# Kernel optimization log

Hardware: AMD Instinct MI355X
Metric: run time of the kernel (lower is better)

The kernel has to match this reference:

```python
import jax, jax.numpy as jnp
import numpy as np

N, E, P = 50000, 800000, 500000
NODE_IN, HIDDEN, EDGE_IN = 128, 256, 16


def setup_inputs() -> dict:
    key = jax.random.key(0)
    ks = jax.random.split(key, 16)
    s = lambda k, shape, fan_in: jax.random.normal(k, shape, jnp.float32) * (1.0 / np.sqrt(fan_in))
    return {
        "x": jax.random.normal(ks[0], (N, NODE_IN), jnp.float32),
        "edge_index": jax.random.randint(ks[1], (2, E), 0, N),
        "edge_u": jax.random.randint(ks[2], (P,), 0, N),
        "edge_v": jax.random.randint(ks[3], (P,), 0, N),
        "edge_attr": jax.random.normal(ks[4], (P, EDGE_IN), jnp.float32),
        "log_exposure": jax.random.normal(ks[5], (P,), jnp.float32),
        # conv1: lin_l (on mean-aggregated neighbors, with bias), lin_r (on root, no bias)
        "Wl1": s(ks[6], (HIDDEN, NODE_IN), NODE_IN),
        "bl1": jnp.zeros((HIDDEN,), jnp.float32),
        "Wr1": s(ks[7], (HIDDEN, NODE_IN), NODE_IN),
        # conv2
        "Wl2": s(ks[8], (HIDDEN, HIDDEN), HIDDEN),
        "bl2": jnp.zeros((HIDDEN,), jnp.float32),
        "Wr2": s(ks[9], (HIDDEN, HIDDEN), HIDDEN),
        # edge MLP: Linear(2*hidden+edge_in, hidden) -> ReLU -> Linear(hidden, 1)
        "W1": s(ks[10], (HIDDEN, 2 * HIDDEN + EDGE_IN), 2 * HIDDEN + EDGE_IN),
        "b1": jnp.zeros((HIDDEN,), jnp.float32),
        "W2": s(ks[11], (1, HIDDEN), HIDDEN),
        "b2": jnp.zeros((1,), jnp.float32),
    }


def sage_conv(x, src, dst, Wl, bl, Wr):
    # PyG SAGEConv, mean aggregation: out = lin_l(mean_{j in N(i)} x_j) + lin_r(x_i)
    n = x.shape[0]
    agg = jax.ops.segment_sum(x[src], dst, num_segments=n)          # [N, F]
    cnt = jax.ops.segment_sum(jnp.ones((src.shape[0],), x.dtype), dst, num_segments=n)
    agg = agg / jnp.maximum(cnt, 1.0)[:, None]
    return agg @ Wl.T + bl + x @ Wr.T


def reference(x, edge_index, edge_u, edge_v, edge_attr, log_exposure,
              Wl1, bl1, Wr1, Wl2, bl2, Wr2, W1, b1, W2, b2):
    src, dst = edge_index[0], edge_index[1]
    # eval mode: dropout is identity
    h = jax.nn.relu(sage_conv(x, src, dst, Wl1, bl1, Wr1))
    h = jax.nn.relu(sage_conv(h, src, dst, Wl2, bl2, Wr2))
    z = jnp.concatenate([h[edge_u], h[edge_v], edge_attr], axis=1)  # [P, 2H+Ein]
    s = (jax.nn.relu(z @ W1.T + b1) @ W2.T + b2)[:, 0]              # [P]
    return log_exposure + s
```

## Files before the change

kernel.cpp:

```cpp
#include <hip/hip_runtime.h>


typedef float f32x4 __attribute__((ext_vector_type(4)));
typedef float f32x2 __attribute__((ext_vector_type(2)));
typedef __bf16 bf16x8 __attribute__((ext_vector_type(8)));

__device__ __forceinline__ unsigned short f2b(float f) {
    unsigned u = __float_as_uint(f);
    u = u + 0x7fffu + ((u >> 16) & 1u);
    return (unsigned short)(u >> 16);
}
__device__ __forceinline__ float b2f(unsigned short s) {
    return __uint_as_float(((unsigned)s) << 16);
}
__device__ __forceinline__ int swz(int r, int g) { return (g + (r >> 1)) & 3; }
__device__ __forceinline__ unsigned char f2f8(float v) {
    return (unsigned char)(__builtin_amdgcn_cvt_pk_fp8_f32(v, v, 0, false) & 0xff);
}


__global__ void k_count(const int* __restrict__ dst, int* __restrict__ cnt, int E) {
    int e = blockIdx.x * 256 + threadIdx.x;
    if (e < E) atomicAdd(&cnt[dst[e]], 1);
}

__global__ __launch_bounds__(1024) void k_scan(int* __restrict__ cnt_cursor,
                                               int* __restrict__ row_ptr, int n) {
    __shared__ int wsum[16];
    __shared__ int carry, wtot;
    int t = threadIdx.x, lane = t & 63, w = t >> 6;
    if (t == 0) carry = 0;
    __syncthreads();
    int nch = (n + 1023) >> 10;
    for (int ch = 0; ch < nch; ++ch) {
        int i = (ch << 10) + t;
        int v = (i < n) ? cnt_cursor[i] : 0;
        int s = v;
        #pragma unroll
        for (int off = 1; off < 64; off <<= 1) {
            int u = __shfl_up(s, off);
            if (lane >= off) s += u;
        }
        if (lane == 63) wsum[w] = s;
        __syncthreads();
        if (t < 16) {
            int vv = wsum[t];
            int s2 = vv;
            #pragma unroll
            for (int off = 1; off < 16; off <<= 1) {
                int u = __shfl_up(s2, off);
                if (t >= off) s2 += u;
            }
            wsum[t] = s2 - vv;
            if (t == 15) wtot = s2;
        }
        __syncthreads();
        int base = carry;
        int incl = s + wsum[w];
        if (i < n) { int ex = base + incl - v; row_ptr[i] = ex; cnt_cursor[i] = ex; }
        __syncthreads();
        if (t == 0) carry = base + wtot;
    }
    __syncthreads();
    if (t == 0) row_ptr[n] = carry;
}

__global__ void k_scatter(const int* __restrict__ src, const int* __restrict__ dst,
                          int* __restrict__ cursor, int* __restrict__ bucket, int E) {
    int e = blockIdx.x * 256 + threadIdx.x;
    if (e < E) {
        int p = atomicAdd(&cursor[dst[e]], 1);
        bucket[p] = src[e];
    }
}


__global__ void k_convert_weights(const float* __restrict__ Wl1, const float* __restrict__ Wr1,
                                  const float* __restrict__ Wl2, const float* __restrict__ Wr2,
                                  const float* __restrict__ W1, const float* __restrict__ b1,
                                  unsigned short* __restrict__ Wc1,
                                  unsigned short* __restrict__ Wc2,
                                  unsigned short* __restrict__ W1g,
                                  unsigned short* __restrict__ WaF) {
    int idx = blockIdx.x * 256 + threadIdx.x;
    if (idx < 65536) {
        int c = idx >> 13, j = (idx >> 5) & 255, kk = idx & 31;
        float v = (c < 4) ? Wl1[j * 128 + c * 32 + kk] : Wr1[j * 128 + (c - 4) * 32 + kk];
        Wc1[idx] = f2b(v);
    } else if (idx < 65536 + 131072) {
        int i2 = idx - 65536;
        int c = i2 >> 13, j = (i2 >> 5) & 255, kk = i2 & 31;
        float v = (c < 8) ? Wl2[j * 256 + c * 32 + kk] : Wr2[j * 256 + (c - 8) * 32 + kk];
        Wc2[i2] = f2b(v);
    } else if (idx < 65536 + 131072 + 131072) {
        int i3 = idx - 65536 - 131072;
        int c = i3 >> 14, j = (i3 >> 5) & 511, kk = i3 & 31;
        float v = (j < 256) ? W1[(size_t)j * 528 + c * 32 + kk]
                            : W1[(size_t)(j - 256) * 528 + 256 + c * 32 + kk];
        W1g[i3] = f2b(v);
    } else if (idx < 65536 + 131072 + 131072 + 8192) {
        int i4 = idx - 65536 - 131072 - 131072;
        int mi = i4 >> 9, l = (i4 >> 3) & 63, j = i4 & 7;
        int m = mi * 16 + (l & 15);
        int k = (l >> 4) * 8 + j;
        float v = (k < 16) ? W1[(size_t)m * 528 + 512 + k] : (k == 16 ? b1[m] : 0.f);
        WaF[i4] = f2b(v);
    }
}

__global__ void k_xconvert(const float* __restrict__ in, unsigned short* __restrict__ xb,
                           unsigned char* __restrict__ xf8, int n) {
    int j = (blockIdx.x * 256 + threadIdx.x) * 2;
    if (j < n) {
        float a = in[j], b = in[j + 1];
        xb[j] = f2b(a); xb[j + 1] = f2b(b);
        unsigned p = __builtin_amdgcn_cvt_pk_fp8_f32(a, b, 0, false);
        *reinterpret_cast<unsigned short*>(xf8 + j) = (unsigned short)(p & 0xffffu);
    }
}


__device__ __forceinline__ void accf8(uint2 v, float* s) {
    f32x2 p0 = __builtin_amdgcn_cvt_pk_f32_fp8(v.x, false);
    f32x2 p1 = __builtin_amdgcn_cvt_pk_f32_fp8(v.x, true);
    f32x2 p2 = __builtin_amdgcn_cvt_pk_f32_fp8(v.y, false);
    f32x2 p3 = __builtin_amdgcn_cvt_pk_f32_fp8(v.y, true);
    s[0] += p0.x; s[1] += p0.y; s[2] += p1.x; s[3] += p1.y;
    s[4] += p2.x; s[5] += p2.y; s[6] += p3.x; s[7] += p3.y;
}

__global__ __launch_bounds__(256) void k_agg_x(const unsigned char* __restrict__ xf8,
                                               const int* __restrict__ row_ptr,
                                               const int* __restrict__ bucket,
                                               unsigned short* __restrict__ agg, int Nn) {
    int node = blockIdx.x * 4 + (threadIdx.x >> 6);
    if (node >= Nn) return;
    int lane = threadIdx.x & 63;
    int q = lane >> 4, c = lane & 15;
    int beg = row_ptr[node], end = row_ptr[node + 1];
    int len = end - beg;
    int lo = beg + ((len * q) >> 2);
    int hi = beg + ((len * (q + 1)) >> 2);
    float s[8] = {0.f,0.f,0.f,0.f,0.f,0.f,0.f,0.f};
    const unsigned char* xp = xf8 + c * 8;
    int e = lo;
    for (; e + 4 <= hi; e += 4) {
        int b0 = bucket[e], b1 = bucket[e + 1], b2 = bucket[e + 2], b3 = bucket[e + 3];
        uint2 v0 = *reinterpret_cast<const uint2*>(xp + (size_t)b0 * 128);
        uint2 v1 = *reinterpret_cast<const uint2*>(xp + (size_t)b1 * 128);
        uint2 v2 = *reinterpret_cast<const uint2*>(xp + (size_t)b2 * 128);
        uint2 v3 = *reinterpret_cast<const uint2*>(xp + (size_t)b3 * 128);
        accf8(v0, s); accf8(v1, s); accf8(v2, s); accf8(v3, s);
    }
    for (; e < hi; ++e)
        accf8(*reinterpret_cast<const uint2*>(xp + (size_t)bucket[e] * 128), s);
    #pragma unroll
    for (int j = 0; j < 8; ++j) {
        s[j] += __shfl_xor(s[j], 16);
        s[j] += __shfl_xor(s[j], 32);
    }
    if (q == 0) {
        float sc = 1.0f / (float)(len > 1 ? len : 1);
        uint4 o;
        o.x = (unsigned)f2b(s[0]*sc) | ((unsigned)f2b(s[1]*sc) << 16);
        o.y = (unsigned)f2b(s[2]*sc) | ((unsigned)f2b(s[3]*sc) << 16);
        o.z = (unsigned)f2b(s[4]*sc) | ((unsigned)f2b(s[5]*sc) << 16);
        o.w = (unsigned)f2b(s[6]*sc) | ((unsigned)f2b(s[7]*sc) << 16);
        *reinterpret_cast<uint4*>(agg + (size_t)node * 128 + c * 8) = o;
    }
}

__global__ __launch_bounds__(256) void k_agg_h(const unsigned char* __restrict__ hf8,
                                               const int* __restrict__ row_ptr,
                                               const int* __restrict__ bucket,
                                               unsigned short* __restrict__ agg, int Nn) {
    int node = blockIdx.x * 4 + (threadIdx.x >> 6);
    if (node >= Nn) return;
    int lane = threadIdx.x & 63;
    int g = lane >> 5, c = lane & 31;
    int beg = row_ptr[node], end = row_ptr[node + 1];
    int len = end - beg;
    int lo = beg + ((len * g) >> 1);
    int hi = beg + ((len * (g + 1)) >> 1);
    float s[8] = {0.f,0.f,0.f,0.f,0.f,0.f,0.f,0.f};
    const unsigned char* hp = hf8 + c * 8;
    int e = lo;
    for (; e + 4 <= hi; e += 4) {
        int b0 = bucket[e], b1 = bucket[e + 1], b2 = bucket[e + 2], b3 = bucket[e + 3];
        uint2 v0 = *reinterpret_cast<const uint2*>(hp + (size_t)b0 * 256);
        uint2 v1 = *reinterpret_cast<const uint2*>(hp + (size_t)b1 * 256);
        uint2 v2 = *reinterpret_cast<const uint2*>(hp + (size_t)b2 * 256);
        uint2 v3 = *reinterpret_cast<const uint2*>(hp + (size_t)b3 * 256);
        accf8(v0, s); accf8(v1, s); accf8(v2, s); accf8(v3, s);
    }
    for (; e < hi; ++e)
        accf8(*reinterpret_cast<const uint2*>(hp + (size_t)bucket[e] * 256), s);
    #pragma unroll
    for (int j = 0; j < 8; ++j) s[j] += __shfl_xor(s[j], 32);
    if (g == 0) {
        float sc = 1.0f / (float)(len > 1 ? len : 1);
        uint4 o;
        o.x = (unsigned)f2b(s[0]*sc) | ((unsigned)f2b(s[1]*sc) << 16);
        o.y = (unsigned)f2b(s[2]*sc) | ((unsigned)f2b(s[3]*sc) << 16);
        o.z = (unsigned)f2b(s[4]*sc) | ((unsigned)f2b(s[5]*sc) << 16);
        o.w = (unsigned)f2b(s[6]*sc) | ((unsigned)f2b(s[7]*sc) << 16);
        *reinterpret_cast<uint4*>(agg + (size_t)node * 256 + c * 8) = o;
    }
}


__global__ __launch_bounds__(256) void k_conv_gemm(const unsigned short* __restrict__ Aagg,
                                                   const unsigned short* __restrict__ Aself,
                                                   const unsigned short* __restrict__ Wck,
                                                   const float* __restrict__ bias,
                                                   unsigned short* __restrict__ Hout,
                                                   unsigned char* __restrict__ Hf8,
                                                   int Nn, int F) {
    __shared__ __align__(16) unsigned short zt[128 * 32];
    __shared__ __align__(16) unsigned short wt[128 * 32];
    const int t = threadIdx.x;
    const int lane = t & 63, w = t >> 6;
    const int wm = w >> 1, wn = w & 1;
    const int node0 = blockIdx.x * 128;
    const int colh = blockIdx.y;
    const int half = F >> 5, nchunks = F >> 4;

    f32x4 acc[4][4];
    #pragma unroll
    for (int i = 0; i < 4; ++i)
        #pragma unroll
        for (int j = 0; j < 4; ++j) acc[i][j] = (f32x4){0.f, 0.f, 0.f, 0.f};

    for (int c = 0; c < nchunks; ++c) {
        __syncthreads();
        const unsigned short* Asrc = (c < half) ? Aagg : Aself;
        const int ccol = ((c < half) ? c : c - half) * 32;
        #pragma unroll
        for (int p = 0; p < 2; ++p) {
            int fc = t + p * 256;
            int row = fc >> 2, seg = fc & 3;
            int node = node0 + row; if (node >= Nn) node = Nn - 1;
            uint4 v = *reinterpret_cast<const uint4*>(Asrc + (size_t)node * F + ccol + seg * 8);
            *reinterpret_cast<uint4*>(&zt[row * 32 + swz(row, seg) * 8]) = v;
        }
        const unsigned short* Wsrc = Wck + ((size_t)c * 256 + colh * 128) * 32;
        #pragma unroll
        for (int p = 0; p < 2; ++p) {
            int fc = t + p * 256;
            int row = fc >> 2, seg = fc & 3;
            *reinterpret_cast<uint4*>(&wt[row * 32 + swz(row, seg) * 8]) =
                *reinterpret_cast<const uint4*>(Wsrc + fc * 8);
        }
        __syncthreads();
        bf16x8 a[4], b[4];
        const int q = lane >> 4;
        #pragma unroll
        for (int mi = 0; mi < 4; ++mi) {
            int R = wm * 64 + mi * 16 + (lane & 15);
            a[mi] = *reinterpret_cast<const bf16x8*>(&zt[R * 32 + swz(R, q) * 8]);
        }
        #pragma unroll
        for (int ni = 0; ni < 4; ++ni) {
            int R = wn * 64 + ni * 16 + (lane & 15);
            b[ni] = *reinterpret_cast<const bf16x8*>(&wt[R * 32 + swz(R, q) * 8]);
        }
        #pragma unroll
        for (int mi = 0; mi < 4; ++mi)
            #pragma unroll
            for (int ni = 0; ni < 4; ++ni)
                acc[mi][ni] = __builtin_amdgcn_mfma_f32_16x16x32_bf16(a[mi], b[ni], acc[mi][ni], 0, 0, 0);
    }

    #pragma unroll
    for (int mi = 0; mi < 4; ++mi)
        #pragma unroll
        for (int ni = 0; ni < 4; ++ni) {
            int col = colh * 128 + wn * 64 + ni * 16 + (lane & 15);
            float bia = bias[col];
            #pragma unroll
            for (int r = 0; r < 4; ++r) {
                int row = node0 + wm * 64 + mi * 16 + ((lane >> 4) << 2) + r;
                if (row < Nn) {
                    float v = acc[mi][ni][r] + bia;
                    v = v > 0.f ? v : 0.f;
                    Hout[(size_t)row * 256 + col] = f2b(v);
                    if (Hf8) Hf8[(size_t)row * 256 + col] = f2f8(v);
                }
            }
        }
}


__global__ __launch_bounds__(256) void k_gemm_g(const unsigned short* __restrict__ A,
                                                const unsigned short* __restrict__ Wck,
                                                unsigned char* __restrict__ Gout,
                                                int Nn) {
    __shared__ __align__(16) unsigned short zt[128 * 32];
    __shared__ __align__(16) unsigned short wt[128 * 32];
    const int t = threadIdx.x;
    const int lane = t & 63, w = t >> 6;
    const int wm = w >> 1, wn = w & 1;
    const int node0 = blockIdx.x * 128;
    const int colg = blockIdx.y;

    f32x4 acc[4][4];
    #pragma unroll
    for (int i = 0; i < 4; ++i)
        #pragma unroll
        for (int j = 0; j < 4; ++j) acc[i][j] = (f32x4){0.f, 0.f, 0.f, 0.f};

    for (int c = 0; c < 8; ++c) {
        __syncthreads();
        #pragma unroll
        for (int p = 0; p < 2; ++p) {
            int fc = t + p * 256;
            int row = fc >> 2, seg = fc & 3;
            int node = node0 + row; if (node >= Nn) node = Nn - 1;
            uint4 v = *reinterpret_cast<const uint4*>(A + (size_t)node * 256 + c * 32 + seg * 8);
            *reinterpret_cast<uint4*>(&zt[row * 32 + swz(row, seg) * 8]) = v;
        }
        const unsigned short* Wsrc = Wck + ((size_t)c * 512 + colg * 128) * 32;
        #pragma unroll
        for (int p = 0; p < 2; ++p) {
            int fc = t + p * 256;
            int row = fc >> 2, seg = fc & 3;
            *reinterpret_cast<uint4*>(&wt[row * 32 + swz(row, seg) * 8]) =
                *reinterpret_cast<const uint4*>(Wsrc + fc * 8);
        }
        __syncthreads();
        bf16x8 a[4], b[4];
        const int q = lane >> 4;
        #pragma unroll
        for (int mi = 0; mi < 4; ++mi) {
            int R = wm * 64 + mi * 16 + (lane & 15);
            a[mi] = *reinterpret_cast<const bf16x8*>(&zt[R * 32 + swz(R, q) * 8]);
        }
        #pragma unroll
        for (int ni = 0; ni < 4; ++ni) {
            int R = wn * 64 + ni * 16 + (lane & 15);
            b[ni] = *reinterpret_cast<const bf16x8*>(&wt[R * 32 + swz(R, q) * 8]);
        }
        #pragma unroll
        for (int mi = 0; mi < 4; ++mi)
            #pragma unroll
            for (int ni = 0; ni < 4; ++ni)
                acc[mi][ni] = __builtin_amdgcn_mfma_f32_16x16x32_bf16(a[mi], b[ni], acc[mi][ni], 0, 0, 0);
    }

    #pragma unroll
    for (int mi = 0; mi < 4; ++mi)
        #pragma unroll
        for (int ni = 0; ni < 4; ++ni) {
            int col = colg * 128 + wn * 64 + ni * 16 + (lane & 15);
            #pragma unroll
            for (int r = 0; r < 4; ++r) {
                int row = node0 + wm * 64 + mi * 16 + ((lane >> 4) << 2) + r;
                if (row < Nn)
                    Gout[(size_t)row * 512 + col] = f2f8(acc[mi][ni][r]);
            }
        }
}


__global__ __launch_bounds__(256, 6) void k_edge(const unsigned char* __restrict__ G2,
                                                 const float* __restrict__ attr,
                                                 const int* __restrict__ eu,
                                                 const int* __restrict__ ev,
                                                 const uint4* __restrict__ WaF,
                                                 const float* __restrict__ W2,
                                                 const float* __restrict__ b2,
                                                 const float* __restrict__ logexp,
                                                 float* __restrict__ out, int P) {
    __shared__ __align__(16) unsigned short attrT[64 * 40];
    __shared__ __align__(16) unsigned char gt[64 * 264];
    __shared__ float w2s[256];
    __shared__ int euv[128];
    const int t = threadIdx.x;
    const int lane = t & 63, w = t >> 6;
    const int base = blockIdx.x * 64;

    {
        int e = t >> 2, seg = t & 3;
        int eg = base + e; if (eg >= P) eg = P - 1;
        const float4 f = *reinterpret_cast<const float4*>(attr + (size_t)eg * 16 + seg * 4);
        uint2 o;
        o.x = (unsigned)f2b(f.x) | ((unsigned)f2b(f.y) << 16);
        o.y = (unsigned)f2b(f.z) | ((unsigned)f2b(f.w) << 16);
        *reinterpret_cast<uint2*>(&attrT[e * 40 + seg * 4]) = o;
    }
    if (t < 64) {
        uint2 z0; z0.x = 0x3f80u; z0.y = 0u;
        *reinterpret_cast<uint2*>(&attrT[t * 40 + 16]) = z0;
        uint2 z1; z1.x = 0u; z1.y = 0u;
        *reinterpret_cast<uint2*>(&attrT[t * 40 + 20]) = z1;
        uint4 z2; z2.x = z2.y = z2.z = z2.w = 0u;
        *reinterpret_cast<uint4*>(&attrT[t * 40 + 24]) = z2;
    }
    if (t < 128) {
        int e = t >> 1;
        int eg = base + e; if (eg >= P) eg = P - 1;
        euv[t] = (t & 1) ? ev[eg] : eu[eg];
    }
    w2s[t] = W2[t];
    __syncthreads();

    const int el = lane & 15, q = lane >> 4;
    const int grow = w * 16 + el;
    const bf16x8 bfrag = *reinterpret_cast<const bf16x8*>(&attrT[grow * 40 + q * 8]);

    float s = 0.f;
    #pragma unroll
    for (int p = 0; p < 2; ++p) {
        {
            const int sub = lane >> 4, c = lane & 15;
            #pragma unroll
            for (int i = 0; i < 4; ++i) {
                int le = w * 16 + i * 4 + sub;
                int u = euv[2 * le], v = euv[2 * le + 1];
                uint2 a = *reinterpret_cast<const uint2*>(G2 + (size_t)u * 512 + p * 128 + c * 8);
                uint2 b = *reinterpret_cast<const uint2*>(G2 + (size_t)v * 512 + 256 + p * 128 + c * 8);
                *reinterpret_cast<uint2*>(&gt[le * 264 + c * 8]) = a;
                *reinterpret_cast<uint2*>(&gt[le * 264 + 128 + c * 8]) = b;
            }
        }
        #pragma unroll
        for (int m = 0; m < 8; ++m) {
            const int mi = p * 8 + m;
            const bf16x8 af = *reinterpret_cast<const bf16x8*>(&WaF[mi * 64 + lane]);
            f32x4 acc = __builtin_amdgcn_mfma_f32_16x16x32_bf16(af, bfrag, (f32x4){0.f,0.f,0.f,0.f}, 0, 0, 0);
            const unsigned gu4 = *reinterpret_cast<const unsigned*>(&gt[grow * 264 + m * 16 + q * 4]);
            const unsigned gv4 = *reinterpret_cast<const unsigned*>(&gt[grow * 264 + 128 + m * 16 + q * 4]);
            const float4 w2v = *reinterpret_cast<const float4*>(&w2s[mi * 16 + q * 4]);
            f32x2 ulo = __builtin_amdgcn_cvt_pk_f32_fp8(gu4, false);
            f32x2 uhi = __builtin_amdgcn_cvt_pk_f32_fp8(gu4, true);
            f32x2 vlo = __builtin_amdgcn_cvt_pk_f32_fp8(gv4, false);
            f32x2 vhi = __builtin_amdgcn_cvt_pk_f32_fp8(gv4, true);
            float y0 = acc[0] + ulo.x + vlo.x;
            float y1 = acc[1] + ulo.y + vlo.y;
            float y2 = acc[2] + uhi.x + vhi.x;
            float y3 = acc[3] + uhi.y + vhi.y;
            s += (y0 > 0.f ? y0 : 0.f) * w2v.x;
            s += (y1 > 0.f ? y1 : 0.f) * w2v.y;
            s += (y2 > 0.f ? y2 : 0.f) * w2v.z;
            s += (y3 > 0.f ? y3 : 0.f) * w2v.w;
        }
        if (p == 0) __syncthreads();
    }
    s += __shfl_xor(s, 16);
    s += __shfl_xor(s, 32);
    int eg = base + grow;
    if (q == 0 && eg < P)
        out[eg] = logexp[eg] + b2[0] + s;
}


extern "C" void kernel_launch(void* const* d_in, const int* in_sizes, int n_in,
                              void* d_out, int out_size, void* d_ws, size_t ws_size,
                              hipStream_t stream) {
    const float* x      = (const float*)d_in[0];
    const int*   eidx   = (const int*)d_in[1];
    const int*   eu     = (const int*)d_in[2];
    const int*   ev     = (const int*)d_in[3];
    const float* attr   = (const float*)d_in[4];
    const float* logexp = (const float*)d_in[5];
    const float* Wl1    = (const float*)d_in[6];
    const float* bl1    = (const float*)d_in[7];
    const float* Wr1    = (const float*)d_in[8];
    const float* Wl2    = (const float*)d_in[9];
    const float* bl2    = (const float*)d_in[10];
    const float* Wr2    = (const float*)d_in[11];
    const float* W1     = (const float*)d_in[12];
    const float* b1     = (const float*)d_in[13];
    const float* W2     = (const float*)d_in[14];
    const float* b2     = (const float*)d_in[15];
    float* out = (float*)d_out;

    const int N = in_sizes[0] / 128;
    const int E = in_sizes[1] / 2;
    const int P = in_sizes[2];
    const int* src = eidx;
    const int* dst = eidx + E;

    char* ws = (char*)d_ws;
    size_t off = 0;
    auto alloc = [&](size_t bytes) -> void* {
        off = (off + 255) & ~(size_t)255;
        void* p = ws + off;
        off += bytes;
        return p;
    };
    int* row_ptr = (int*)alloc((size_t)(N + 1) * 4);
    int* cursor  = (int*)alloc((size_t)N * 4);
    int* bucket  = (int*)alloc((size_t)E * 4);
    unsigned short* h1 = (unsigned short*)alloc((size_t)N * 256 * 2);
    unsigned short* h2 = (unsigned short*)alloc((size_t)N * 256 * 2);
    char* shared_base = (char*)alloc((size_t)N * 512 * 2);
    unsigned short* xb   = (unsigned short*)shared_base;
    unsigned short* agg1 = (unsigned short*)(shared_base + (size_t)N * 128 * 2);
    unsigned short* agg2 = (unsigned short*)(shared_base + (size_t)N * 256 * 2);
    unsigned char*  G2f8 = (unsigned char*)shared_base;
    unsigned char* xf8  = (unsigned char*)alloc((size_t)N * 128);
    unsigned char* h1f8 = (unsigned char*)alloc((size_t)N * 256);
    unsigned short* Wc1  = (unsigned short*)alloc((size_t)65536 * 2);
    unsigned short* Wc2  = (unsigned short*)alloc((size_t)131072 * 2);
    unsigned short* W1g  = (unsigned short*)alloc((size_t)131072 * 2);
    unsigned short* WaF  = (unsigned short*)alloc((size_t)8192 * 2);

    hipMemsetAsync(cursor, 0, (size_t)N * 4, stream);
    k_count<<<(E + 255) / 256, 256, 0, stream>>>(dst, cursor, E);
    k_scan<<<1, 1024, 0, stream>>>(cursor, row_ptr, N);
    k_scatter<<<(E + 255) / 256, 256, 0, stream>>>(src, dst, cursor, bucket, E);
    k_convert_weights<<<(65536 + 131072 + 131072 + 8192 + 255) / 256, 256, 0, stream>>>(
        Wl1, Wr1, Wl2, Wr2, W1, b1, Wc1, Wc2, W1g, WaF);
    k_xconvert<<<(N * 64 + 255) / 256, 256, 0, stream>>>(x, xb, xf8, N * 128);

    k_agg_x<<<(N + 3) / 4, 256, 0, stream>>>(xf8, row_ptr, bucket, agg1, N);
    dim3 gconv((N + 127) / 128, 2);
    k_conv_gemm<<<gconv, 256, 0, stream>>>(agg1, xb, Wc1, bl1, h1, h1f8, N, 128);
    k_agg_h<<<(N + 3) / 4, 256, 0, stream>>>(h1f8, row_ptr, bucket, agg2, N);
    k_conv_gemm<<<gconv, 256, 0, stream>>>(agg2, h1, Wc2, bl2, h2, (unsigned char*)nullptr, N, 256);

    dim3 gg((N + 127) / 128, 4);
    k_gemm_g<<<gg, 256, 0, stream>>>(h2, W1g, G2f8, N);
    k_edge<<<(P + 63) / 64, 256, 0, stream>>>(G2f8, attr, eu, ev, (const uint4*)WaF,
                                              W2, b2, logexp, out, P);
}
```

Measured before the change: 479.6 us.

## Fuse setup kernels and stage GEMM tiles via direct global-to-LDS loads

Merges the edge-count, weight-conversion and x-conversion kernels into one launch that dispatches on block index, saving two kernel launches. In both GEMM kernels, the register round-trip for A and W tiles is replaced with global_load_lds 16-byte transfers straight into shared memory. Because those loads write LDS in lane order, the XOR-style swizzle is dropped and fragment reads use a linear layout. This risks LDS bank conflicts on the MFMA operand reads, and correctness depends on the builtin's per-wave LDS placement matching the row*32+q*8 indexing.

```diff
diff --git a/kernel.cpp b/kernel.cpp
--- a/kernel.cpp
+++ b/kernel.cpp
@@ -17,12 +17,61 @@
 __device__ __forceinline__ unsigned char f2f8(float v) {
     return (unsigned char)(__builtin_amdgcn_cvt_pk_fp8_f32(v, v, 0, false) & 0xff);
 }
-
-
-__global__ void k_count(const int* __restrict__ dst, int* __restrict__ cnt, int E) {
-    int e = blockIdx.x * 256 + threadIdx.x;
-    if (e < E) atomicAdd(&cnt[dst[e]], 1);
-}
+__device__ __forceinline__ void gld16(const void* g, void* l) {
+    __builtin_amdgcn_global_load_lds((const __attribute__((address_space(1))) void*)g,
+                                     (__attribute__((address_space(3))) void*)l, 16, 0, 0);
+}
+
+
+__global__ void k_setup(const int* __restrict__ dst, int* __restrict__ cnt, int E,
+                        const float* __restrict__ Wl1, const float* __restrict__ Wr1,
+                        const float* __restrict__ Wl2, const float* __restrict__ Wr2,
+                        const float* __restrict__ W1, const float* __restrict__ b1,
+                        unsigned short* __restrict__ Wc1, unsigned short* __restrict__ Wc2,
+                        unsigned short* __restrict__ W1g, unsigned short* __restrict__ WaF,
+                        const float* __restrict__ x, unsigned short* __restrict__ xb,
+                        unsigned char* __restrict__ xf8, int nx,
+                        int nbCount, int nbConv) {
+    int b = blockIdx.x;
+    if (b < nbCount) {
+        int e = b * 256 + threadIdx.x;
+        if (e < E) atomicAdd(&cnt[dst[e]], 1);
+    } else if (b < nbCount + nbConv) {
+        int idx = (b - nbCount) * 256 + threadIdx.x;
+        if (idx < 65536) {
+            int c = idx >> 13, j = (idx >> 5) & 255, kk = idx & 31;
+            float v = (c < 4) ? Wl1[j * 128 + c * 32 + kk] : Wr1[j * 128 + (c - 4) * 32 + kk];
+            Wc1[idx] = f2b(v);
+        } else if (idx < 65536 + 131072) {
+            int i2 = idx - 65536;
+            int c = i2 >> 13, j = (i2 >> 5) & 255, kk = i2 & 31;
+            float v = (c < 8) ? Wl2[j * 256 + c * 32 + kk] : Wr2[j * 256 + (c - 8) * 32 + kk];
+            Wc2[i2] = f2b(v);
+        } else if (idx < 65536 + 131072 + 131072) {
+            int i3 = idx - 65536 - 131072;
+            int c = i3 >> 14, j = (i3 >> 5) & 511, kk = i3 & 31;
+            float v = (j < 256) ? W1[(size_t)j * 528 + c * 32 + kk]
+                                : W1[(size_t)(j - 256) * 528 + 256 + c * 32 + kk];
+            W1g[i3] = f2b(v);
+        } else if (idx < 65536 + 131072 + 131072 + 8192) {
+            int i4 = idx - 65536 - 131072 - 131072;
+            int mi = i4 >> 9, l = (i4 >> 3) & 63, j = i4 & 7;
+            int m = mi * 16 + (l & 15);
+            int k = (l >> 4) * 8 + j;
+            float v = (k < 16) ? W1[(size_t)m * 528 + 512 + k] : (k == 16 ? b1[m] : 0.f);
+            WaF[i4] = f2b(v);
+        }
+    } else {
+        int j = ((b - nbCount - nbConv) * 256 + threadIdx.x) * 2;
+        if (j < nx) {
+            float a = x[j], c = x[j + 1];
+            xb[j] = f2b(a); xb[j + 1] = f2b(c);
+            unsigned p = __builtin_amdgcn_cvt_pk_fp8_f32(a, c, 0, false);
+            *reinterpret_cast<unsigned short*>(xf8 + j) = (unsigned short)(p & 0xffffu);
+        }
+    }
+}
+
 
 __global__ __launch_bounds__(1024) void k_scan(int* __restrict__ cnt_cursor,
                                                int* __restrict__ row_ptr, int n) {
@@ -71,51 +120,6 @@
     if (e < E) {
         int p = atomicAdd(&cursor[dst[e]], 1);
         bucket[p] = src[e];
-    }
-}
-
-
-__global__ void k_convert_weights(const float* __restrict__ Wl1, const float* __restrict__ Wr1,
-                                  const float* __restrict__ Wl2, const float* __restrict__ Wr2,
-                                  const float* __restrict__ W1, const float* __restrict__ b1,
-                                  unsigned short* __restrict__ Wc1,
-                                  unsigned short* __restrict__ Wc2,
-                                  unsigned short* __restrict__ W1g,
-                                  unsigned short* __restrict__ WaF) {
-    int idx = blockIdx.x * 256 + threadIdx.x;
-    if (idx < 65536) {
-        int c = idx >> 13, j = (idx >> 5) & 255, kk = idx & 31;
-        float v = (c < 4) ? Wl1[j * 128 + c * 32 + kk] : Wr1[j * 128 + (c - 4) * 32 + kk];
-        Wc1[idx] = f2b(v);
-    } else if (idx < 65536 + 131072) {
-        int i2 = idx - 65536;
-        int c = i2 >> 13, j = (i2 >> 5) & 255, kk = i2 & 31;
-        float v = (c < 8) ? Wl2[j * 256 + c * 32 + kk] : Wr2[j * 256 + (c - 8) * 32 + kk];
-        Wc2[i2] = f2b(v);
-    } else if (idx < 65536 + 131072 + 131072) {
-        int i3 = idx - 65536 - 131072;
-        int c = i3 >> 14, j = (i3 >> 5) & 511, kk = i3 & 31;
-        float v = (j < 256) ? W1[(size_t)j * 528 + c * 32 + kk]
-                            : W1[(size_t)(j - 256) * 528 + 256 + c * 32 + kk];
-        W1g[i3] = f2b(v);
-    } else if (idx < 65536 + 131072 + 131072 + 8192) {
-        int i4 = idx - 65536 - 131072 - 131072;
-        int mi = i4 >> 9, l = (i4 >> 3) & 63, j = i4 & 7;
-        int m = mi * 16 + (l & 15);
-        int k = (l >> 4) * 8 + j;
-        float v = (k < 16) ? W1[(size_t)m * 528 + 512 + k] : (k == 16 ? b1[m] : 0.f);
-        WaF[i4] = f2b(v);
-    }
-}
-
-__global__ void k_xconvert(const float* __restrict__ in, unsigned short* __restrict__ xb,
-                           unsigned char* __restrict__ xf8, int n) {
-    int j = (blockIdx.x * 256 + threadIdx.x) * 2;
-    if (j < n) {
-        float a = in[j], b = in[j + 1];
-        xb[j] = f2b(a); xb[j + 1] = f2b(b);
-        unsigned p = __builtin_amdgcn_cvt_pk_fp8_f32(a, b, 0, false);
-        *reinterpret_cast<unsigned short*>(xf8 + j) = (unsigned short)(p & 0xffffu);
     }
 }
 
@@ -236,20 +240,17 @@
         const unsigned short* Asrc = (c < half) ? Aagg : Aself;
         const int ccol = ((c < half) ? c : c - half) * 32;
         #pragma unroll
-        for (int p = 0; p < 2; ++p) {
-            int fc = t + p * 256;
+        for (int j = 0; j < 2; ++j) {
+            int fc = (w * 2 + j) * 64 + lane;
             int row = fc >> 2, seg = fc & 3;
             int node = node0 + row; if (node >= Nn) node = Nn - 1;
-            uint4 v = *reinterpret_cast<const uint4*>(Asrc + (size_t)node * F + ccol + seg * 8);
-            *reinterpret_cast<uint4*>(&zt[row * 32 + swz(row, seg) * 8]) = v;
+            gld16(Asrc + (size_t)node * F + ccol + seg * 8, &zt[(w * 2 + j) * 512]);
         }
         const unsigned short* Wsrc = Wck + ((size_t)c * 256 + colh * 128) * 32;
         #pragma unroll
-        for (int p = 0; p < 2; ++p) {
-            int fc = t + p * 256;
-            int row = fc >> 2, seg = fc & 3;
-            *reinterpret_cast<uint4*>(&wt[row * 32 + swz(row, seg) * 8]) =
-                *reinterpret_cast<const uint4*>(Wsrc + fc * 8);
+        for (int j = 0; j < 2; ++j) {
+            int fc = (w * 2 + j) * 64 + lane;
+            gld16(Wsrc + fc * 8, &wt[(w * 2 + j) * 512]);
         }
         __syncthreads();
         bf16x8 a[4], b[4];
@@ -257,12 +258,12 @@
         #pragma unroll
         for (int mi = 0; mi < 4; ++mi) {
             int R = wm * 64 + mi * 16 + (lane & 15);
-            a[mi] = *reinterpret_cast<const bf16x8*>(&zt[R * 32 + swz(R, q) * 8]);
+            a[mi] = *reinterpret_cast<const bf16x8*>(&zt[R * 32 + q * 8]);
         }
         #pragma unroll
         for (int ni = 0; ni < 4; ++ni) {
             int R = wn * 64 + ni * 16 + (lane & 15);
-            b[ni] = *reinterpret_cast<const bf16x8*>(&wt[R * 32 + swz(R, q) * 8]);
+            b[ni] = *reinterpret_cast<const bf16x8*>(&wt[R * 32 + q * 8]);
         }
         #pragma unroll
         for (int mi = 0; mi < 4; ++mi)
@@ -312,20 +313,17 @@
     for (int c = 0; c < 8; ++c) {
         __syncthreads();
         #pragma unroll
-        for (int p = 0; p < 2; ++p) {
-            int fc = t + p * 256;
+        for (int j = 0; j < 2; ++j) {
+            int fc = (w * 2 + j) * 64 + lane;
             int row = fc >> 2, seg = fc & 3;
             int node = node0 + row; if (node >= Nn) node = Nn - 1;
-            uint4 v = *reinterpret_cast<const uint4*>(A + (size_t)node * 256 + c * 32 + seg * 8);
-            *reinterpret_cast<uint4*>(&zt[row * 32 + swz(row, seg) * 8]) = v;
+            gld16(A + (size_t)node * 256 + c * 32 + seg * 8, &zt[(w * 2 + j) * 512]);
         }
         const unsigned short* Wsrc = Wck + ((size_t)c * 512 + colg * 128) * 32;
         #pragma unroll
-        for (int p = 0; p < 2; ++p) {
-            int fc = t + p * 256;
-            int row = fc >> 2, seg = fc & 3;
-            *reinterpret_cast<uint4*>(&wt[row * 32 + swz(row, seg) * 8]) =
-                *reinterpret_cast<const uint4*>(Wsrc + fc * 8);
+        for (int j = 0; j < 2; ++j) {
+            int fc = (w * 2 + j) * 64 + lane;
+            gld16(Wsrc + fc * 8, &wt[(w * 2 + j) * 512]);
         }
         __syncthreads();
         bf16x8 a[4], b[4];
@@ -333,12 +331,12 @@
         #pragma unroll
         for (int mi = 0; mi < 4; ++mi) {
             int R = wm * 64 + mi * 16 + (lane & 15);
-            a[mi] = *reinterpret_cast<const bf16x8*>(&zt[R * 32 + swz(R, q) * 8]);
+            a[mi] = *reinterpret_cast<const bf16x8*>(&zt[R * 32 + q * 8]);
         }
         #pragma unroll
         for (int ni = 0; ni < 4; ++ni) {
             int R = wn * 64 + ni * 16 + (lane & 15);
-            b[ni] = *reinterpret_cast<const bf16x8*>(&wt[R * 32 + swz(R, q) * 8]);
+            b[ni] = *reinterpret_cast<const bf16x8*>(&wt[R * 32 + q * 8]);
         }
         #pragma unroll
         for (int mi = 0; mi < 4; ++mi)
@@ -507,12 +505,14 @@
     unsigned short* WaF  = (unsigned short*)alloc((size_t)8192 * 2);
 
     hipMemsetAsync(cursor, 0, (size_t)N * 4, stream);
-    k_count<<<(E + 255) / 256, 256, 0, stream>>>(dst, cursor, E);
+    const int nbCount = (E + 255) / 256;
+    const int nbConv  = (65536 + 131072 + 131072 + 8192 + 255) / 256;
+    const int nbX     = (N * 64 + 255) / 256;
+    k_setup<<<nbCount + nbConv + nbX, 256, 0, stream>>>(
+        dst, cursor, E, Wl1, Wr1, Wl2, Wr2, W1, b1, Wc1, Wc2, W1g, WaF,
+        x, xb, xf8, N * 128, nbCount, nbConv);
     k_scan<<<1, 1024, 0, stream>>>(cursor, row_ptr, N);
     k_scatter<<<(E + 255) / 256, 256, 0, stream>>>(src, dst, cursor, bucket, E);
-    k_convert_weights<<<(65536 + 131072 + 131072 + 8192 + 255) / 256, 256, 0, stream>>>(
-        Wl1, Wr1, Wl2, Wr2, W1, b1, Wc1, Wc2, W1g, WaF);
-    k_xconvert<<<(N * 64 + 255) / 256, 256, 0, stream>>>(x, xb, xf8, N * 128);
 
     k_agg_x<<<(N + 3) / 4, 256, 0, stream>>>(xf8, row_ptr, bucket, agg1, N);
     dim3 gconv((N + 127) / 128, 2);
```

Result: faster. 466.1 us (-2.8%).
